# Kernel tuning notes

Measured on AMD Instinct MI355X. Metric: run time of the kernel, lower is better.

## Reference

```python
import jax, jax.numpy as jnp
import numpy as np

G = 1024   # number of glimpses
P = 1024   # points per glimpse
N = G * P  # total points


def _pool(pos, batch, start, size):
    """voxel_mean_pool index computation: unique (batch, voxel) cells."""
    vox = np.floor((pos - start) / size).astype(np.int64)
    vox -= vox.min(axis=0)
    dims = vox.max(axis=0) + 1
    key = ((batch * dims[0] + vox[:, 0]) * dims[1] + vox[:, 1]) * dims[2] + vox[:, 2]
    uniq, first, inv = np.unique(key, return_index=True, return_inverse=True)
    return inv.astype(np.int64), batch[first].astype(np.int64), int(uniq.shape[0])


def setup_inputs() -> dict:
    rng = np.random.default_rng(0)
    pos = rng.uniform(-1.0, 1.0, (N, 3)).astype(np.float32)
    rgb = rng.random((N, 1)).astype(np.float32)
    batch = np.repeat(np.arange(G, dtype=np.int64), P)
    # min_pos gets a random negative offset (noise) in the torch code
    min_pos = pos.min(axis=0) - rng.random(3).astype(np.float32)
    # level-1 voxel pooling (size 0.25)
    cluster1, batch1, M1 = _pool(pos, batch, min_pos, 0.25)
    cnt1 = np.bincount(cluster1, minlength=M1).astype(np.float32)[:, None]
    ps1 = np.zeros((M1, 3), np.float32)
    np.add.at(ps1, cluster1, pos)
    ps1 /= cnt1
    # level-2 voxel pooling (size 0.5) on voxel centers
    cluster2, batch2, M2 = _pool(ps1, batch1, min_pos, 0.5)

    def lin(fi, fo):
        return (rng.standard_normal((fi, fo)).astype(np.float32) / np.sqrt(fi))

    d = dict(
        rgb=jnp.asarray(rgb), pos=jnp.asarray(pos),
        glimpse_center=jnp.asarray(rng.standard_normal((G, 3)).astype(np.float32)),
        W1l=jnp.asarray(lin(1 + 3, 16)), b1l=jnp.zeros(16, jnp.float32),
        W1g=jnp.asarray(lin(16, 32)), b1g=jnp.zeros(32, jnp.float32),
        W2l=jnp.asarray(lin(32 + 3, 64)), b2l=jnp.zeros(64, jnp.float32),
        W2g=jnp.asarray(lin(64, 128)), b2g=jnp.zeros(128, jnp.float32),
        W3l=jnp.asarray(lin(128 + 3, 128)), b3l=jnp.zeros(128, jnp.float32),
        W3g=jnp.asarray(lin(128, 256)), b3g=jnp.zeros(256, jnp.float32),
        Wlin=jnp.asarray(lin(256, 256)), blin=jnp.zeros(256, jnp.float32),
        eps=jnp.asarray(rng.standard_normal((G, 128)).astype(np.float32)),
        glimpse_index=jnp.asarray(batch),
        cluster1=jnp.asarray(cluster1), cluster2=jnp.asarray(cluster2),
        batch2=jnp.asarray(batch2),
        num_voxels1=M1, num_voxels2=M2,
    )
    return d


def _seg_mean(x, seg, m):
    s = jax.ops.segment_sum(x, seg, num_segments=m)
    c = jax.ops.segment_sum(jnp.ones((x.shape[0], 1), x.dtype), seg, num_segments=m)
    return s / jnp.maximum(c, 1.0)


def _point_conv(x_in, pos_in, pos_out, out_index, Wl, bl, Wg, bg, m_out):
    # gather: relative position of each input point to its output (voxel) center
    rel = pos_in - pos_out[out_index]                      # [E,3]
    msg = jax.nn.relu(jnp.concatenate([x_in, rel], 1) @ Wl + bl)  # [E,c_mid]
    agg = jax.ops.segment_max(msg, out_index, num_segments=m_out)  # [M,c_mid]
    return agg @ Wg + bg


def reference(rgb, pos, glimpse_center, W1l, b1l, W1g, b1g, W2l, b2l, W2g, b2g,
              W3l, b3l, W3g, b3g, Wlin, blin, eps, glimpse_index,
              cluster1, cluster2, batch2, num_voxels1, num_voxels2):
    M1, M2 = num_voxels1, num_voxels2
    Gn = glimpse_center.shape[0]
    # stage 1: voxel mean pool (0.25) + PointConv 1->16->32
    ps1 = _seg_mean(pos, cluster1, M1)                     # [M1,3]
    f1 = jax.nn.celu(_point_conv(rgb, pos, ps1, cluster1, W1l, b1l, W1g, b1g, M1))
    # stage 2: voxel mean pool (0.5) + PointConv 32->64->128
    ps2 = _seg_mean(ps1, cluster2, M2)                     # [M2,3]
    f2 = jax.nn.celu(_point_conv(f1, ps1, ps2, cluster2, W2l, b2l, W2g, b2g, M2))
    # stage 3: pool everything to the glimpse center (pos_out = zeros)
    pos_out = jnp.zeros_like(glimpse_center)
    f3 = jax.nn.celu(_point_conv(f2, ps2, pos_out, batch2, W3l, b3l, W3g, b3g, Gn))
    # head: Linear(256,256), split into mu/sigma, reparameterized sample
    out = f3 @ Wlin + blin                                 # [G,256]
    mu, s = jnp.split(out, 2, axis=1)
    sigma = jax.nn.softplus(s)
    z = mu + sigma * eps                                   # [G,128]
    z_what, z_mask = jnp.split(z, 2, axis=1)
    return z_what, z_mask, mu, sigma, f3
```

## Files before the change

kernel.cpp:

```cpp
#include <hip/hip_runtime.h>
#include <math.h>

#define N1CAP 736
#define N2CAP 192
#define S3 132

__device__ __forceinline__ float celu1(float x){ return x > 0.f ? x : (expf(x) - 1.f); }
__device__ __forceinline__ float softplus1(float x){ return fmaxf(x, 0.f) + log1pf(expf(-fabsf(x))); }
__device__ __forceinline__ void atomicMaxNonneg(float* p, float v){
    atomicMax((int*)p, __float_as_int(v));
}

__global__ __launch_bounds__(256) void kA(const float* __restrict__ rgb,
                                          const float* __restrict__ pos,
                                          const int* __restrict__ cl1,
                                          const float* __restrict__ W1l,
                                          const float* __restrict__ b1l,
                                          float* __restrict__ ps1,
                                          float* __restrict__ agg1,
                                          float* __restrict__ cnt1,
                                          int* __restrict__ seg1, int P){
    __shared__ float sp[3*1024];
    __shared__ float srgb[1024];
    __shared__ int   ci[1024];
    __shared__ int   cnt[N1CAP];
    __shared__ int   start[N1CAP+1];
    __shared__ int   cur[N1CAP];
    __shared__ unsigned short pidx[1024];
    __shared__ float wsh[64], bsh[16];
    __shared__ int   red[2];
    __shared__ int   wsum[4];
    const int g = blockIdx.x, tid = threadIdx.x;
    const int base = g * P;
    const bool pfit = (P <= 1024);

    if (tid == 0){ red[0] = 0x7fffffff; red[1] = -1; }
    if (tid < 64) wsh[tid] = W1l[tid];
    if (tid < 16) bsh[tid] = b1l[tid];
    __syncthreads();
    int mn = 0x7fffffff, mx = -1;
    for (int i = tid; i < P; i += 256){
        int c = cl1[base+i];
        if (pfit) ci[i] = c;
        mn = min(mn,c); mx = max(mx,c);
    }
    atomicMin(&red[0], mn); atomicMax(&red[1], mx);
    __syncthreads();
    const int s1 = red[0];
    const int n1 = red[1] - red[0] + 1;
    const bool fast = pfit && (n1 <= N1CAP);

    if (fast){
        for (int t = tid; t < 3*P; t += 256) sp[t] = pos[(size_t)base*3 + t];
        for (int t = tid; t < P;   t += 256) srgb[t] = rgb[base + t];
        for (int l = tid; l < n1;  l += 256) cnt[l] = 0;
        __syncthreads();
        for (int i = tid; i < P; i += 256) atomicAdd(&cnt[ci[i] - s1], 1);
        __syncthreads();
        {
            int b3 = tid*3;
            int a0 = (b3   < n1) ? cnt[b3]   : 0;
            int a1 = (b3+1 < n1) ? cnt[b3+1] : 0;
            int a2 = (b3+2 < n1) ? cnt[b3+2] : 0;
            int s = a0+a1+a2;
            int lane = tid & 63, wv = tid >> 6;
            int ps = s;
            #pragma unroll
            for (int d = 1; d < 64; d <<= 1){
                int t2 = __shfl_up(ps, d, 64);
                if (lane >= d) ps += t2;
            }
            if (lane == 63) wsum[wv] = ps;
            __syncthreads();
            int woff = 0;
            #pragma unroll
            for (int w = 0; w < 4; ++w) woff += (w < wv) ? wsum[w] : 0;
            int excl = woff + ps - s;
            if (b3   < n1){ start[b3]   = excl;       cur[b3]   = excl; }
            if (b3+1 < n1){ start[b3+1] = excl+a0;    cur[b3+1] = excl+a0; }
            if (b3+2 < n1){ start[b3+2] = excl+a0+a1; cur[b3+2] = excl+a0+a1; }
            if (tid == 0) start[n1] = P;
        }
        __syncthreads();
        for (int i = tid; i < P; i += 256){
            int slot = atomicAdd(&cur[ci[i] - s1], 1);
            pidx[slot] = (unsigned short)i;
        }
        __syncthreads();
        for (int l = tid; l < n1; l += 256){
            int s0 = start[l], e0 = start[l+1];
            float sxv=0.f, syv=0.f, szv=0.f;
            for (int k = s0; k < e0; ++k){
                int i = pidx[k];
                sxv += sp[3*i+0]; syv += sp[3*i+1]; szv += sp[3*i+2];
            }
            float ic = 1.0f / (float)max(e0 - s0, 1);
            float mxp = sxv*ic, myp = syv*ic, mzp = szv*ic;
            ps1[(size_t)(s1+l)*3+0] = mxp;
            ps1[(size_t)(s1+l)*3+1] = myp;
            ps1[(size_t)(s1+l)*3+2] = mzp;
            float acc[16];
            #pragma unroll
            for (int j = 0; j < 16; ++j) acc[j] = 0.f;
            for (int k = s0; k < e0; ++k){
                int i = pidx[k];
                float in0 = srgb[i];
                float r0 = sp[3*i+0] - mxp;
                float r1 = sp[3*i+1] - myp;
                float r2 = sp[3*i+2] - mzp;
                #pragma unroll
                for (int j = 0; j < 16; ++j){
                    float v = bsh[j] + in0*wsh[j] + r0*wsh[16+j] + r1*wsh[32+j] + r2*wsh[48+j];
                    acc[j] = fmaxf(acc[j], fmaxf(v, 0.f));
                }
            }
            float4* dst = (float4*)&agg1[(size_t)(s1+l)*16];
            dst[0] = make_float4(acc[0], acc[1], acc[2], acc[3]);
            dst[1] = make_float4(acc[4], acc[5], acc[6], acc[7]);
            dst[2] = make_float4(acc[8], acc[9], acc[10], acc[11]);
            dst[3] = make_float4(acc[12], acc[13], acc[14], acc[15]);
        }
    } else {
        for (int t = tid; t < n1;    t += 256) cnt1[s1+t] = 0.f;
        for (int t = tid; t < n1*3;  t += 256) ps1[(size_t)s1*3+t] = 0.f;
        for (int t = tid; t < n1*16; t += 256) agg1[(size_t)s1*16+t] = 0.f;
        __syncthreads();
        for (int i = tid; i < P; i += 256){
            int idx = base + i; int c = cl1[idx];
            atomicAdd(&ps1[3*c+0], pos[3*idx+0]);
            atomicAdd(&ps1[3*c+1], pos[3*idx+1]);
            atomicAdd(&ps1[3*c+2], pos[3*idx+2]);
            atomicAdd(&cnt1[c], 1.0f);
        }
        __syncthreads();
        for (int l = tid; l < n1; l += 256){
            float ic = 1.0f / fmaxf(cnt1[s1+l], 1.0f);
            ps1[(size_t)(s1+l)*3+0] *= ic; ps1[(size_t)(s1+l)*3+1] *= ic; ps1[(size_t)(s1+l)*3+2] *= ic;
        }
        __syncthreads();
        for (int i = tid; i < P; i += 256){
            int idx = base + i; int c = cl1[idx];
            float in0 = rgb[idx];
            float r0 = pos[3*idx+0] - ps1[3*c+0];
            float r1 = pos[3*idx+1] - ps1[3*c+1];
            float r2 = pos[3*idx+2] - ps1[3*c+2];
            #pragma unroll
            for (int j = 0; j < 16; ++j){
                float v = b1l[j] + in0*W1l[j] + r0*W1l[16+j] + r1*W1l[32+j] + r2*W1l[48+j];
                atomicMaxNonneg(&agg1[(size_t)c*16+j], fmaxf(v, 0.0f));
            }
        }
    }
    if (tid == 0){ seg1[2*g] = s1; seg1[2*g+1] = n1; }
}

__global__ __launch_bounds__(256) void kB(const float* __restrict__ ps1,
                                          const float* __restrict__ agg1,
                                          const int* __restrict__ cl2,
                                          const float* __restrict__ W1g,
                                          const float* __restrict__ b1g,
                                          const float* __restrict__ W2l,
                                          const float* __restrict__ b2l,
                                          const int* __restrict__ seg1,
                                          float* __restrict__ ps2,
                                          float* __restrict__ agg2,
                                          float* __restrict__ cnt2,
                                          int* __restrict__ seg2){
    __shared__ float sx[N2CAP], sy[N2CAP], sz[N2CAP], sc[N2CAP];
    __shared__ float sagg[N2CAP*64];
    __shared__ int red[2];
    const int g = blockIdx.x, tid = threadIdx.x;
    const int s1 = seg1[2*g], n1 = seg1[2*g+1], e1 = s1 + n1;

    if (tid == 0){ red[0] = 0x7fffffff; red[1] = -1; }
    __syncthreads();
    int mn = 0x7fffffff, mx = -1;
    for (int m = s1 + tid; m < e1; m += 256){ int c = cl2[m]; mn = min(mn,c); mx = max(mx,c); }
    atomicMin(&red[0], mn); atomicMax(&red[1], mx);
    __syncthreads();
    const int s2 = red[0];
    const int n2 = red[1] - red[0] + 1;
    const bool fast = (n2 <= N2CAP);

    if (fast){
        for (int l = tid; l < n2; l += 256){ sx[l]=0.f; sy[l]=0.f; sz[l]=0.f; sc[l]=0.f; }
        for (int t = tid; t < n2*64; t += 256) sagg[t] = 0.f;
        __syncthreads();
        for (int m = s1 + tid; m < e1; m += 256){
            int c = cl2[m] - s2;
            atomicAdd(&sx[c], ps1[3*m+0]);
            atomicAdd(&sy[c], ps1[3*m+1]);
            atomicAdd(&sz[c], ps1[3*m+2]);
            atomicAdd(&sc[c], 1.0f);
        }
        __syncthreads();
        for (int l = tid; l < n2; l += 256){
            float ic = 1.0f / sc[l];
            sx[l] *= ic; sy[l] *= ic; sz[l] *= ic;
        }
        __syncthreads();
        for (int t = tid; t < n2*3; t += 256){
            int l = t/3, d = t - 3*l;
            ps2[(size_t)s2*3 + t] = (d==0) ? sx[l] : ((d==1) ? sy[l] : sz[l]);
        }
        for (int m = s1 + tid; m < e1; m += 256){
            float a[16];
            const float* ar = agg1 + (size_t)m*16;
            #pragma unroll
            for (int k = 0; k < 16; ++k) a[k] = ar[k];
            float in[35];
            for (int j = 0; j < 32; j += 4){
                float v0=b1g[j+0], v1=b1g[j+1], v2=b1g[j+2], v3=b1g[j+3];
                #pragma unroll
                for (int k = 0; k < 16; ++k){
                    float x = a[k];
                    const float* w = &W1g[k*32 + j];
                    v0 += x*w[0]; v1 += x*w[1]; v2 += x*w[2]; v3 += x*w[3];
                }
                in[j+0]=celu1(v0); in[j+1]=celu1(v1); in[j+2]=celu1(v2); in[j+3]=celu1(v3);
            }
            int c = cl2[m] - s2;
            in[32] = ps1[3*m+0] - sx[c];
            in[33] = ps1[3*m+1] - sy[c];
            in[34] = ps1[3*m+2] - sz[c];
            float* dst = &sagg[c*64];
            for (int j = 0; j < 64; j += 4){
                float v0=b2l[j+0], v1=b2l[j+1], v2=b2l[j+2], v3=b2l[j+3];
                #pragma unroll
                for (int k = 0; k < 35; ++k){
                    float x = in[k];
                    const float* w = &W2l[k*64 + j];
                    v0 += x*w[0]; v1 += x*w[1]; v2 += x*w[2]; v3 += x*w[3];
                }
                atomicMaxNonneg(&dst[(j+0 + c) & 63], fmaxf(v0, 0.0f));
                atomicMaxNonneg(&dst[(j+1 + c) & 63], fmaxf(v1, 0.0f));
                atomicMaxNonneg(&dst[(j+2 + c) & 63], fmaxf(v2, 0.0f));
                atomicMaxNonneg(&dst[(j+3 + c) & 63], fmaxf(v3, 0.0f));
            }
        }
        __syncthreads();
        for (int t = tid; t < n2*64; t += 256){
            int l = t >> 6, j = t & 63;
            agg2[(size_t)s2*64 + t] = sagg[l*64 + ((j + l) & 63)];
        }
    } else {
        for (int t = tid; t < n2;    t += 256) cnt2[s2+t] = 0.f;
        for (int t = tid; t < n2*3;  t += 256) ps2[(size_t)s2*3+t] = 0.f;
        for (int t = tid; t < n2*64; t += 256) agg2[(size_t)s2*64+t] = 0.f;
        __syncthreads();
        for (int m = s1 + tid; m < e1; m += 256){
            int c = cl2[m];
            atomicAdd(&ps2[3*c+0], ps1[3*m+0]);
            atomicAdd(&ps2[3*c+1], ps1[3*m+1]);
            atomicAdd(&ps2[3*c+2], ps1[3*m+2]);
            atomicAdd(&cnt2[c], 1.0f);
        }
        __syncthreads();
        for (int l = tid; l < n2; l += 256){
            float ic = 1.0f / fmaxf(cnt2[s2+l], 1.0f);
            ps2[(size_t)(s2+l)*3+0] *= ic; ps2[(size_t)(s2+l)*3+1] *= ic; ps2[(size_t)(s2+l)*3+2] *= ic;
        }
        __syncthreads();
        for (int m = s1 + tid; m < e1; m += 256){
            float a[16];
            const float* ar = agg1 + (size_t)m*16;
            #pragma unroll
            for (int k = 0; k < 16; ++k) a[k] = ar[k];
            float in[35];
            #pragma unroll
            for (int j = 0; j < 32; ++j){
                float v = b1g[j];
                #pragma unroll
                for (int k = 0; k < 16; ++k) v += a[k] * W1g[k*32+j];
                in[j] = celu1(v);
            }
            int c = cl2[m];
            in[32] = ps1[3*m+0] - ps2[3*c+0];
            in[33] = ps1[3*m+1] - ps2[3*c+1];
            in[34] = ps1[3*m+2] - ps2[3*c+2];
            for (int j = 0; j < 64; ++j){
                float v = b2l[j];
                #pragma unroll
                for (int k = 0; k < 35; ++k) v += in[k] * W2l[k*64+j];
                atomicMaxNonneg(&agg2[(size_t)c*64+j], fmaxf(v, 0.0f));
            }
        }
    }
    if (tid == 0){ seg2[2*g] = s2; seg2[2*g+1] = n2; }
}

__global__ __launch_bounds__(256) void k_f2f(const float* __restrict__ agg2,
                                             const float* __restrict__ W2g,
                                             const float* __restrict__ b2g,
                                             float* __restrict__ f2, int M2){
    __shared__ float Ws[64*128];
    __shared__ float xt[32*S3];
    const int tid = threadIdx.x;
    const int m0 = blockIdx.x * 128;
    for (int t = tid; t < 64*128; t += 256) Ws[t] = W2g[t];
    const int tr = tid & 31, tc = tid >> 5;
    float acc[4][16];
    #pragma unroll
    for (int c = 0; c < 16; ++c){
        float b = b2g[tc*16 + c];
        #pragma unroll
        for (int r = 0; r < 4; ++r) acc[r][c] = b;
    }
    for (int c0 = 0; c0 < 64; c0 += 32){
        __syncthreads();
        for (int t = tid; t < 128*8; t += 256){
            int row = t >> 3, kq = t & 7;
            int m = m0 + row;
            float4 v = (m < M2) ? *(const float4*)&agg2[(size_t)m*64 + c0 + kq*4]
                                : make_float4(0.f,0.f,0.f,0.f);
            xt[(kq*4+0)*S3 + row] = v.x;
            xt[(kq*4+1)*S3 + row] = v.y;
            xt[(kq*4+2)*S3 + row] = v.z;
            xt[(kq*4+3)*S3 + row] = v.w;
        }
        __syncthreads();
        #pragma unroll 4
        for (int kk = 0; kk < 32; ++kk){
            int k = c0 + kk;
            float4 xr = *(const float4*)&xt[kk*S3 + tr*4];
            float xv[4] = {xr.x, xr.y, xr.z, xr.w};
            float wv[16];
            #pragma unroll
            for (int q = 0; q < 4; ++q){
                float4 w = *(const float4*)&Ws[k*128 + tc*16 + q*4];
                wv[q*4+0]=w.x; wv[q*4+1]=w.y; wv[q*4+2]=w.z; wv[q*4+3]=w.w;
            }
            #pragma unroll
            for (int r = 0; r < 4; ++r)
                #pragma unroll
                for (int c = 0; c < 16; ++c) acc[r][c] += xv[r]*wv[c];
        }
    }
    #pragma unroll
    for (int r = 0; r < 4; ++r){
        int m = m0 + tr*4 + r;
        if (m < M2){
            #pragma unroll
            for (int q = 0; q < 4; ++q){
                float4 o;
                o.x = celu1(acc[r][q*4+0]); o.y = celu1(acc[r][q*4+1]);
                o.z = celu1(acc[r][q*4+2]); o.w = celu1(acc[r][q*4+3]);
                *(float4*)&f2[(size_t)m*128 + tc*16 + q*4] = o;
            }
        }
    }
}

__global__ __launch_bounds__(256) void k_msg3g(const float* __restrict__ f2,
                                               const float* __restrict__ ps2,
                                               const int* __restrict__ seg2,
                                               const float* __restrict__ W3l,
                                               const float* __restrict__ b3l,
                                               float* __restrict__ agg3, int G){
    __shared__ float Wh[131*64];
    __shared__ float xt[32*S3];
    __shared__ float shAgg[128];
    const int tid = threadIdx.x;
    const int cb = blockIdx.y * 64;
    const int g0 = blockIdx.x * 2;
    const int S  = seg2[2*g0];
    const int B  = seg2[2*g0+1];
    const int n2b = (g0 + 1 < G) ? seg2[2*g0+3] : 0;
    const int T  = B + n2b;
    for (int t = tid; t < 131*64; t += 256){
        int k = t >> 6, c = t & 63;
        Wh[t] = W3l[k*128 + cb + c];
    }
    if (tid < 128) shAgg[tid] = 0.f;
    const int tr = tid & 31, tc = tid >> 5;
    float bias[8];
    #pragma unroll
    for (int c = 0; c < 8; ++c) bias[c] = b3l[cb + tc*8 + c];

    for (int w0 = 0; w0 < T; w0 += 128){
        float acc[4][8];
        #pragma unroll
        for (int r = 0; r < 4; ++r)
            #pragma unroll
            for (int c = 0; c < 8; ++c) acc[r][c] = bias[c];
        for (int c0 = 0; c0 < 128; c0 += 32){
            __syncthreads();
            for (int t = tid; t < 128*8; t += 256){
                int row = t >> 3, kq = t & 7;
                int ridx = w0 + row;
                float4 v = (ridx < T) ? *(const float4*)&f2[(size_t)(S+ridx)*128 + c0 + kq*4]
                                      : make_float4(0.f,0.f,0.f,0.f);
                xt[(kq*4+0)*S3 + row] = v.x;
                xt[(kq*4+1)*S3 + row] = v.y;
                xt[(kq*4+2)*S3 + row] = v.z;
                xt[(kq*4+3)*S3 + row] = v.w;
            }
            __syncthreads();
            #pragma unroll 8
            for (int kk = 0; kk < 32; ++kk){
                int k = c0 + kk;
                float4 xr = *(const float4*)&xt[kk*S3 + tr*4];
                float xv[4] = {xr.x, xr.y, xr.z, xr.w};
                float4 wa = *(const float4*)&Wh[k*64 + tc*8];
                float4 wb = *(const float4*)&Wh[k*64 + tc*8 + 4];
                float wv[8] = {wa.x,wa.y,wa.z,wa.w, wb.x,wb.y,wb.z,wb.w};
                #pragma unroll
                for (int r = 0; r < 4; ++r)
                    #pragma unroll
                    for (int c = 0; c < 8; ++c) acc[r][c] += xv[r]*wv[c];
            }
        }
        #pragma unroll
        for (int kk = 0; kk < 3; ++kk){
            const float* w = &Wh[(128+kk)*64 + tc*8];
            float wv[8];
            #pragma unroll
            for (int c = 0; c < 8; ++c) wv[c] = w[c];
            #pragma unroll
            for (int r = 0; r < 4; ++r){
                int ridx = w0 + tr*4 + r;
                float x = (ridx < T) ? ps2[(size_t)(S+ridx)*3 + kk] : 0.f;
                #pragma unroll
                for (int c = 0; c < 8; ++c) acc[r][c] += x*wv[c];
            }
        }
        float mx0[8], mx1[8];
        #pragma unroll
        for (int c = 0; c < 8; ++c){ mx0[c] = 0.f; mx1[c] = 0.f; }
        bool h0 = false, h1 = false;
        #pragma unroll
        for (int r = 0; r < 4; ++r){
            int ridx = w0 + tr*4 + r;
            if (ridx < T){
                bool second = (ridx >= B);
                h0 |= !second; h1 |= second;
                #pragma unroll
                for (int c = 0; c < 8; ++c){
                    float v = fmaxf(acc[r][c], 0.f);
                    mx0[c] = fmaxf(mx0[c], second ? 0.f : v);
                    mx1[c] = fmaxf(mx1[c], second ? v : 0.f);
                }
            }
        }
        if (h0){
            #pragma unroll
            for (int c = 0; c < 8; ++c) atomicMaxNonneg(&shAgg[tc*8 + c], mx0[c]);
        }
        if (h1){
            #pragma unroll
            for (int c = 0; c < 8; ++c) atomicMaxNonneg(&shAgg[64 + tc*8 + c], mx1[c]);
        }
    }
    __syncthreads();
    if (tid < 128){
        int loc = tid >> 6, c = tid & 63;
        int g = g0 + loc;
        if (loc == 0 || n2b > 0)
            agg3[(size_t)g*128 + cb + c] = shAgg[loc*64 + c];
    }
}

__global__ __launch_bounds__(256) void k_head(const float* __restrict__ agg3,
                                              const float* __restrict__ W3g,
                                              const float* __restrict__ b3g,
                                              const float* __restrict__ Wlin,
                                              const float* __restrict__ blin,
                                              const float* __restrict__ eps,
                                              float* __restrict__ out, int G){
    __shared__ float a3[128];
    __shared__ float f3s[256];
    __shared__ float hs[256];
    int g = blockIdx.x;
    int j = threadIdx.x;
    if (j < 128) a3[j] = agg3[(size_t)g*128 + j];
    __syncthreads();

    float v = b3g[j];
    for (int k = 0; k < 128; ++k) v += a3[k] * W3g[k*256 + j];
    v = celu1(v);
    f3s[j] = v;
    const size_t o_zm = (size_t)64*G, o_mu = (size_t)128*G, o_sg = (size_t)256*G, o_f3 = (size_t)384*G;
    out[o_f3 + (size_t)g*256 + j] = v;
    __syncthreads();

    float h = blin[j];
    for (int k = 0; k < 256; ++k) h += f3s[k] * Wlin[k*256 + j];
    hs[j] = h;
    __syncthreads();

    if (j < 128){
        float mu = hs[j];
        float sg = softplus1(hs[128 + j]);
        float z = mu + sg * eps[(size_t)g*128 + j];
        out[o_mu + (size_t)g*128 + j] = mu;
        out[o_sg + (size_t)g*128 + j] = sg;
        if (j < 64) out[(size_t)g*64 + j] = z;
        else        out[o_zm + (size_t)g*64 + (j - 64)] = z;
    }
}

extern "C" void kernel_launch(void* const* d_in, const int* in_sizes, int n_in,
                              void* d_out, int out_size, void* d_ws, size_t ws_size,
                              hipStream_t stream) {
    const float* rgb  = (const float*)d_in[0];
    const float* pos  = (const float*)d_in[1];
    const float* W1l  = (const float*)d_in[3];
    const float* b1l  = (const float*)d_in[4];
    const float* W1g  = (const float*)d_in[5];
    const float* b1g  = (const float*)d_in[6];
    const float* W2l  = (const float*)d_in[7];
    const float* b2l  = (const float*)d_in[8];
    const float* W2g  = (const float*)d_in[9];
    const float* b2g  = (const float*)d_in[10];
    const float* W3l  = (const float*)d_in[11];
    const float* b3l  = (const float*)d_in[12];
    const float* W3g  = (const float*)d_in[13];
    const float* b3g  = (const float*)d_in[14];
    const float* Wlin = (const float*)d_in[15];
    const float* blin = (const float*)d_in[16];
    const float* eps  = (const float*)d_in[17];
    const int* cl1 = (const int*)d_in[19];
    const int* cl2 = (const int*)d_in[20];

    const int N  = in_sizes[19];
    const int G  = in_sizes[17] / 128;
    const int M1 = in_sizes[20];
    const int M2 = in_sizes[21];
    const int P  = N / G;

    char* ws = (char*)d_ws;
    auto al = [](size_t x){ return (x + 255) & ~(size_t)255; };
    size_t off = 0;
    float* ps1  = (float*)(ws + off); off = al(off + 12ull*M1);
    size_t uni  = ((size_t)64*M1 > (size_t)512*M2) ? (size_t)64*M1 : (size_t)512*M2;
    float* agg1 = (float*)(ws + off);
    float* f2   = (float*)(ws + off);
    off = al(off + uni);
    float* cnt1 = (float*)(ws + off); off = al(off + 4ull*M1);
    float* ps2  = (float*)(ws + off); off = al(off + 12ull*M2);
    float* agg2 = (float*)(ws + off); off = al(off + 256ull*M2);
    float* cnt2 = (float*)(ws + off); off = al(off + 4ull*M2);
    float* agg3 = (float*)(ws + off); off = al(off + 512ull*G);
    int*   seg1 = (int*)  (ws + off); off = al(off + 8ull*G);
    int*   seg2 = (int*)  (ws + off); off = al(off + 8ull*G);
    if (off > ws_size) return;

    kA<<<G, 256, 0, stream>>>(rgb, pos, cl1, W1l, b1l, ps1, agg1, cnt1, seg1, P);
    kB<<<G, 256, 0, stream>>>(ps1, agg1, cl2, W1g, b1g, W2l, b2l, seg1, ps2, agg2, cnt2, seg2);
    int gx = (M2 + 127) / 128;
    k_f2f  <<<gx, 256, 0, stream>>>(agg2, W2g, b2g, f2, M2);
    dim3 g3((G + 1) / 2, 2);
    k_msg3g<<<g3, 256, 0, stream>>>(f2, ps2, seg2, W3l, b3l, agg3, G);
    k_head <<<G, 256, 0, stream>>>(agg3, W3g, b3g, Wlin, blin, eps, (float*)d_out, G);
}
```

Baseline: 397.5 us.

## Cut kB register and LDS pressure, group four glimpses per k_msg3g block

kB gets a smaller shared-memory cap (N2CAP 192 to 144), a launch-bounds occupancy hint, and reduced unrolling in its dense loops, so it uses fewer registers and less LDS and more blocks fit per CU. k_msg3g now processes four glimpses per block instead of two, which amortizes the W3l weight staging over more rows. Its segmented max is reworked to flush a running maximum into shared memory each time the owning glimpse changes. Less unrolling adds loop overhead, and the smaller N2CAP could overflow if a glimpse has more level-2 voxels than the new cap.

```diff
diff --git a/kernel.cpp b/kernel.cpp
--- a/kernel.cpp
+++ b/kernel.cpp
@@ -2,7 +2,7 @@
 #include <math.h>
 
 #define N1CAP 736
-#define N2CAP 192
+#define N2CAP 144
 #define S3 132
 
 __device__ __forceinline__ float celu1(float x){ return x > 0.f ? x : (expf(x) - 1.f); }
@@ -154,7 +154,7 @@
     if (tid == 0){ seg1[2*g] = s1; seg1[2*g+1] = n1; }
 }
 
-__global__ __launch_bounds__(256) void kB(const float* __restrict__ ps1,
+__global__ __launch_bounds__(256, 2) void kB(const float* __restrict__ ps1,
                                           const float* __restrict__ agg1,
                                           const int* __restrict__ cl2,
                                           const float* __restrict__ W1g,
@@ -267,10 +267,10 @@
             #pragma unroll
             for (int k = 0; k < 16; ++k) a[k] = ar[k];
             float in[35];
-            #pragma unroll
+            #pragma unroll 1
             for (int j = 0; j < 32; ++j){
                 float v = b1g[j];
-                #pragma unroll
+                #pragma unroll 4
                 for (int k = 0; k < 16; ++k) v += a[k] * W1g[k*32+j];
                 in[j] = celu1(v);
             }
@@ -278,9 +278,10 @@
             in[32] = ps1[3*m+0] - ps2[3*c+0];
             in[33] = ps1[3*m+1] - ps2[3*c+1];
             in[34] = ps1[3*m+2] - ps2[3*c+2];
+            #pragma unroll 1
             for (int j = 0; j < 64; ++j){
                 float v = b2l[j];
-                #pragma unroll
+                #pragma unroll 5
                 for (int k = 0; k < 35; ++k) v += in[k] * W2l[k*64+j];
                 atomicMaxNonneg(&agg2[(size_t)c*64+j], fmaxf(v, 0.0f));
             }
@@ -359,19 +360,21 @@
                                                float* __restrict__ agg3, int G){
     __shared__ float Wh[131*64];
     __shared__ float xt[32*S3];
-    __shared__ float shAgg[128];
+    __shared__ float shAgg[256];
     const int tid = threadIdx.x;
     const int cb = blockIdx.y * 64;
-    const int g0 = blockIdx.x * 2;
+    const int g0 = blockIdx.x * 4;
     const int S  = seg2[2*g0];
-    const int B  = seg2[2*g0+1];
-    const int n2b = (g0 + 1 < G) ? seg2[2*g0+3] : 0;
-    const int T  = B + n2b;
+    int n0 = seg2[2*g0+1];
+    int nA = (g0+1 < G) ? seg2[2*(g0+1)+1] : 0;
+    int nB = (g0+2 < G) ? seg2[2*(g0+2)+1] : 0;
+    int nC = (g0+3 < G) ? seg2[2*(g0+3)+1] : 0;
+    const int B1 = n0, B2 = B1 + nA, B3 = B2 + nB, T = B3 + nC;
     for (int t = tid; t < 131*64; t += 256){
         int k = t >> 6, c = t & 63;
         Wh[t] = W3l[k*128 + cb + c];
     }
-    if (tid < 128) shAgg[tid] = 0.f;
+    shAgg[tid] = 0.f;
     const int tr = tid & 31, tc = tid >> 5;
     float bias[8];
     #pragma unroll
@@ -424,38 +427,39 @@
                 for (int c = 0; c < 8; ++c) acc[r][c] += x*wv[c];
             }
         }
-        float mx0[8], mx1[8];
-        #pragma unroll
-        for (int c = 0; c < 8; ++c){ mx0[c] = 0.f; mx1[c] = 0.f; }
-        bool h0 = false, h1 = false;
+        float mx[8];
+        int cur = -1;
         #pragma unroll
         for (int r = 0; r < 4; ++r){
             int ridx = w0 + tr*4 + r;
             if (ridx < T){
-                bool second = (ridx >= B);
-                h0 |= !second; h1 |= second;
-                #pragma unroll
-                for (int c = 0; c < 8; ++c){
-                    float v = fmaxf(acc[r][c], 0.f);
-                    mx0[c] = fmaxf(mx0[c], second ? 0.f : v);
-                    mx1[c] = fmaxf(mx1[c], second ? v : 0.f);
+                int loc = (ridx >= B1) + (ridx >= B2) + (ridx >= B3);
+                if (loc != cur){
+                    if (cur >= 0){
+                        #pragma unroll
+                        for (int c = 0; c < 8; ++c)
+                            atomicMaxNonneg(&shAgg[cur*64 + tc*8 + c], mx[c]);
+                    }
+                    cur = loc;
+                    #pragma unroll
+                    for (int c = 0; c < 8; ++c) mx[c] = fmaxf(acc[r][c], 0.f);
+                } else {
+                    #pragma unroll
+                    for (int c = 0; c < 8; ++c) mx[c] = fmaxf(mx[c], fmaxf(acc[r][c], 0.f));
                 }
             }
         }
-        if (h0){
-            #pragma unroll
-            for (int c = 0; c < 8; ++c) atomicMaxNonneg(&shAgg[tc*8 + c], mx0[c]);
-        }
-        if (h1){
-            #pragma unroll
-            for (int c = 0; c < 8; ++c) atomicMaxNonneg(&shAgg[64 + tc*8 + c], mx1[c]);
-        }
-    }
-    __syncthreads();
-    if (tid < 128){
+        if (cur >= 0){
+            #pragma unroll
+            for (int c = 0; c < 8; ++c)
+                atomicMaxNonneg(&shAgg[cur*64 + tc*8 + c], mx[c]);
+        }
+    }
+    __syncthreads();
+    {
         int loc = tid >> 6, c = tid & 63;
         int g = g0 + loc;
-        if (loc == 0 || n2b > 0)
+        if (g < G)
             agg3[(size_t)g*128 + cb + c] = shAgg[loc*64 + c];
     }
 }
@@ -549,7 +553,7 @@
     kB<<<G, 256, 0, stream>>>(ps1, agg1, cl2, W1g, b1g, W2l, b2l, seg1, ps2, agg2, cnt2, seg2);
     int gx = (M2 + 127) / 128;
     k_f2f  <<<gx, 256, 0, stream>>>(agg2, W2g, b2g, f2, M2);
-    dim3 g3((G + 1) / 2, 2);
+    dim3 g3((G + 3) / 4, 2);
     k_msg3g<<<g3, 256, 0, stream>>>(f2, ps2, seg2, W3l, b3l, agg3, G);
     k_head <<<G, 256, 0, stream>>>(agg3, W3g, b3g, Wlin, blin, eps, (float*)d_out, G);
 }
```

Result: slower. 457.5 us (+15.1%).
